# Kernel tuning notes

Hardware: AMD Instinct MI355X
Metric: run time of the kernel (lower is better)

The kernel has to match this reference:

```python
import jax, jax.numpy as jnp
import numpy as np

NU, NM = 100000, 20000   # users, merchants
FU, FM = 64, 32          # input feature dims
H = 128                  # hidden_channels
E = 1000000              # edges per edge type
ET = 500000              # target edges


def setup_inputs() -> dict:
    key = jax.random.key(0)
    ks = jax.random.split(key, 24)
    f = lambda i, shape: jax.random.normal(ks[i], shape, jnp.float32) * 0.05
    ri = lambda i, n, hi: jax.random.randint(ks[i], (n,), 0, hi)
    return {
        'x_user': f(0, (NU, FU)),
        'x_merchant': f(1, (NM, FM)),
        'row_um': ri(2, E, NU), 'col_um': ri(3, E, NM),
        'row_mu': ri(4, E, NM), 'col_mu': ri(5, E, NU),
        'row_t': ri(6, ET, NU), 'col_t': ri(7, ET, NM),
        'W1l_um': f(8, (FU, H)), 'W1r_um': f(9, (FM, H)), 'b1_um': jnp.zeros((H,), jnp.float32),
        'W1l_mu': f(10, (FM, H)), 'W1r_mu': f(11, (FU, H)), 'b1_mu': jnp.zeros((H,), jnp.float32),
        'W2l_um': f(12, (H, H)), 'W2r_um': f(13, (H, H)), 'b2_um': jnp.zeros((H,), jnp.float32),
        'W2l_mu': f(14, (H, H)), 'W2r_mu': f(15, (H, H)), 'b2_mu': jnp.zeros((H,), jnp.float32),
        'Wc1': f(16, (2 * H, H)), 'bc1': jnp.zeros((H,), jnp.float32),
        'Wc2': f(17, (H, 1)), 'bc2': jnp.zeros((1,), jnp.float32),
    }


def _sage(x_src, x_dst, row, col, Wl, Wr, b, n_dst):
    # PyG SAGEConv (aggr='mean'): lin_l(mean of neighbor msgs) + lin_r(root) + bias
    deg = jax.ops.segment_sum(jnp.ones(row.shape[0], x_src.dtype), col, num_segments=n_dst)
    agg = jax.ops.segment_sum(x_src[row], col, num_segments=n_dst)
    agg = agg / jnp.maximum(deg, 1.0)[:, None]
    return agg @ Wl + x_dst @ Wr + b


def reference(x_user, x_merchant, row_um, col_um, row_mu, col_mu, row_t, col_t,
              W1l_um, W1r_um, b1_um, W1l_mu, W1r_mu, b1_mu,
              W2l_um, W2r_um, b2_um, W2l_mu, W2r_mu, b2_mu,
              Wc1, bc1, Wc2, bc2):
    # Layer 1 (each dest type receives exactly one edge type -> hetero-mean is identity)
    h_m = jax.nn.relu(_sage(x_user, x_merchant, row_um, col_um, W1l_um, W1r_um, b1_um, NM))
    h_u = jax.nn.relu(_sage(x_merchant, x_user, row_mu, col_mu, W1l_mu, W1r_mu, b1_mu, NU))
    # Layer 2 (no activation)
    z_m = _sage(h_u, h_m, row_um, col_um, W2l_um, W2r_um, b2_um, NM)
    z_u = _sage(h_m, h_u, row_mu, col_mu, W2l_mu, W2r_mu, b2_mu, NU)
    # Edge classifier: gather sender ('user') / receiver ('merchant'), concat, MLP
    z = jnp.concatenate([z_u[row_t], z_m[col_t]], axis=-1)  # [ET, 2H]
    h = jax.nn.relu(z @ Wc1 + bc1)
    return (h @ Wc2 + bc2).reshape(-1)
```

## Files before the change

kernel.cpp:

```cpp
#include <hip/hip_runtime.h>
#include <hip/hip_bf16.h>

#define NUV 100000
#define NMV 20000
#define NEV 1000000
#define ETV 500000

#define CHK 8192
#define NCH 123
#define WNM 5000
#define WNU 25000
#define NCA 5
#define NCB 25
#define HGRID 1954
#define MBLK 5000
#define G1MB 625
#define G2MB 313

typedef unsigned short u16;
typedef unsigned int u32;
typedef __attribute__((ext_vector_type(8))) short s16x8;
typedef __attribute__((ext_vector_type(4))) float f32x4;
typedef __attribute__((ext_vector_type(4))) unsigned short u16x4;
typedef __attribute__((ext_vector_type(4))) unsigned int u32x4;

__device__ inline u16 bf16r(float f) {
  u32 b = __builtin_bit_cast(u32, f);
  u32 r = b + 0x7fffu + ((b >> 16) & 1u);
  return (u16)(r >> 16);
}
__device__ inline float bflo(u32 v) { return __builtin_bit_cast(float, v << 16); }
__device__ inline float bfhi(u32 v) { return __builtin_bit_cast(float, v & 0xffff0000u); }

#define GLOAD_LDS16(src, dst) \
  __builtin_amdgcn_global_load_lds((const __attribute__((address_space(1))) void*)(src), \
                                   (__attribute__((address_space(3))) void*)(dst), 16, 0, 0)

__global__ __launch_bounds__(512) void k_hist_lds(
    const int* __restrict__ col_um, u32* __restrict__ rankp_um, u32* __restrict__ cnt_um,
    const int* __restrict__ col_mu, u32* __restrict__ rankp_mu, u32* __restrict__ cnt_mu) {
  __shared__ u32 hist[WNU];
  int bid = blockIdx.x, tid = threadIdx.x;
  bool um = bid < NCH;
  const int* col = um ? col_um : col_mu;
  u32* rankp = um ? rankp_um : rankp_mu;
  u32* cntp = um ? cnt_um : cnt_mu;
  int Wn = um ? WNM : WNU;
  int blk = um ? bid : bid - NCH;
  int e0 = blk * CHK;
  for (int i = tid; i < Wn; i += 512) hist[i] = 0;
  __syncthreads();
  #pragma unroll
  for (int it = 0; it < CHK / 2048; ++it) {
    int li = e0 + (it * 512 + tid) * 4;
    if (li < NEV) {
      int4 c = *(const int4*)(col + li);
      int cc[4] = {c.x, c.y, c.z, c.w};
      u32 pk = 0;
      #pragma unroll
      for (int q = 0; q < 4; ++q) {
        int d = cc[q];
        int sh = 8 * (d & 3);
        u32 old = atomicAdd(&hist[d >> 2], 1u << sh);
        pk |= ((old >> sh) & 0xFFu) << (8 * q);
      }
      rankp[li >> 2] = pk;
    }
  }
  __syncthreads();
  u32* dst = cntp + (size_t)blk * Wn;
  for (int i = tid; i < Wn; i += 512) dst[i] = hist[i];
}

__global__ __launch_bounds__(1024) void k_scan_s1(
    const u32* __restrict__ cnt_um, u32* __restrict__ pre_um,
    const u32* __restrict__ cnt_mu, u32* __restrict__ pre_mu,
    int* __restrict__ T, int* __restrict__ bsum) {
  int b = blockIdx.x;
  const u32* cnt; u32* pre; int Wn; int w0; int* Tout;
  if (b < NCA) { cnt = cnt_um; pre = pre_um; Wn = WNM; w0 = b * 1024; Tout = T; }
  else         { cnt = cnt_mu; pre = pre_mu; Wn = WNU; w0 = (b - NCA) * 1024; Tout = T + NMV; }
  __shared__ int wsum[16];
  int tid = threadIdx.x, lane = tid & 63, w = tid >> 6;
  int wd = w0 + tid;
  int r0 = 0, r1 = 0, r2 = 0, r3 = 0;
  if (wd < Wn) {
    #pragma unroll 4
    for (int bb = 0; bb < NCH; ++bb) {
      u32 v = cnt[(size_t)bb * Wn + wd];
      pre[(size_t)bb * Wn + wd] =
          (u32)r0 | ((u32)r1 << 8) | ((u32)r2 << 16) | ((u32)r3 << 24);
      r0 += v & 0xFF; r1 += (v >> 8) & 0xFF; r2 += (v >> 16) & 0xFF; r3 += (v >> 24) & 0xFF;
    }
    *(int4*)(Tout + wd * 4) = make_int4(r0, r1, r2, r3);
  }
  int tot = r0 + r1 + r2 + r3;
  #pragma unroll
  for (int d = 1; d < 64; d <<= 1) tot += __shfl_xor(tot, d);
  if (lane == 0) wsum[w] = tot;
  __syncthreads();
  if (tid == 0) {
    int a = 0;
    #pragma unroll
    for (int j = 0; j < 16; ++j) a += wsum[j];
    bsum[b] = a;
  }
}

__global__ __launch_bounds__(128) void k_scan_s2(int* __restrict__ bsum,
                                                 int* __restrict__ off_um, int* __restrict__ off_mu) {
  int tid = threadIdx.x;
  int wv = tid >> 6, lane = tid & 63;
  if (wv == 0) {
    int v = (lane < NCA) ? bsum[lane] : 0;
    int s = v;
    #pragma unroll
    for (int d = 1; d < 64; d <<= 1) { int t = __shfl_up(s, d); if (lane >= d) s += t; }
    if (lane < NCA) bsum[lane] = s - v;
  } else {
    int v = (lane < NCB) ? bsum[NCA + lane] : 0;
    int s = v;
    #pragma unroll
    for (int d = 1; d < 64; d <<= 1) { int t = __shfl_up(s, d); if (lane >= d) s += t; }
    if (lane < NCB) bsum[NCA + lane] = s - v;
  }
  if (tid == 0) { off_um[NMV] = NEV; off_mu[NUV] = NEV; }
}

__global__ __launch_bounds__(1024) void k_scan_s3(int* __restrict__ off_um,
                                                  int* __restrict__ off_mu,
                                                  const int* __restrict__ T,
                                                  const int* __restrict__ bsum) {
  int b = blockIdx.x;
  int N; int c0; int* offo; const int* Tin;
  if (b < NCA) { N = NMV; c0 = b * 4096; offo = off_um; Tin = T; }
  else         { N = NUV; c0 = (b - NCA) * 4096; offo = off_mu; Tin = T + NMV; }
  int carry = bsum[b];
  __shared__ int wsum[16];
  int tid = threadIdx.x, lane = tid & 63, w = tid >> 6;
  int c = c0 + tid * 4;
  int4 tv = make_int4(0, 0, 0, 0);
  if (c < N) tv = *(const int4*)(Tin + c);
  int p1 = tv.x + tv.y, p2 = p1 + tv.z, p3 = p2 + tv.w;
  int sc = p3;
  #pragma unroll
  for (int d = 1; d < 64; d <<= 1) { int t = __shfl_up(sc, d); if (lane >= d) sc += t; }
  if (lane == 63) wsum[w] = sc;
  __syncthreads();
  if (w == 0 && lane < 16) {
    int ws_ = wsum[lane];
    #pragma unroll
    for (int d = 1; d < 16; d <<= 1) { int t = __shfl_up(ws_, d, 16); if (lane >= d) ws_ += t; }
    wsum[lane] = ws_;
  }
  __syncthreads();
  int ex = sc - p3 + (w ? wsum[w - 1] : 0) + carry;
  if (c < N) *(int4*)(offo + c) = make_int4(ex, ex + tv.x, ex + p1, ex + p2);
}

__global__ __launch_bounds__(256) void k_scatter3(
    const int* __restrict__ col_um, const int* __restrict__ row_um,
    const u32* __restrict__ rankp_um, const u32* __restrict__ pre_um,
    const int* __restrict__ off_um, int* __restrict__ srow_um,
    const int* __restrict__ col_mu, const int* __restrict__ row_mu,
    const u32* __restrict__ rankp_mu, const u32* __restrict__ pre_mu,
    const int* __restrict__ off_mu, int* __restrict__ srow_mu) {
  int i = (blockIdx.x * 256 + threadIdx.x) * 4;
  if (i >= 2 * NEV) return;
  bool um = i < NEV;
  const int* col = um ? col_um : col_mu;
  const int* row = um ? row_um : row_mu;
  const u32* rankp = um ? rankp_um : rankp_mu;
  const u32* pre = um ? pre_um : pre_mu;
  const int* off = um ? off_um : off_mu;
  int Wn = um ? WNM : WNU;
  int* srow = um ? srow_um : srow_mu;
  int lo = um ? i : i - NEV;
  int blk = lo >> 13;
  const u32* prep = pre + (size_t)blk * Wn;
  int4 c = *(const int4*)(col + lo);
  int4 rr = *(const int4*)(row + lo);
  u32 pk = rankp[lo >> 2];
  int cc[4] = {c.x, c.y, c.z, c.w}, rv[4] = {rr.x, rr.y, rr.z, rr.w};
  #pragma unroll
  for (int q = 0; q < 4; ++q) {
    int d = cc[q];
    int prefix = (int)((prep[d >> 2] >> (8 * (d & 3))) & 0xFF);
    int rank = (int)((pk >> (8 * q)) & 0xFF);
    srow[off[d] + prefix + rank] = rv[q];
  }
}

__global__ __launch_bounds__(256) void k_xub(const float* __restrict__ in, u32* __restrict__ o, int n8) {
  int stride = gridDim.x * 256;
  for (int i = blockIdx.x * 256 + threadIdx.x; i < n8; i += stride) {
    float4 a = *(const float4*)(in + (size_t)i * 8);
    float4 b = *(const float4*)(in + (size_t)i * 8 + 4);
    u32x4 r;
    r[0] = (u32)bf16r(a.x) | ((u32)bf16r(a.y) << 16);
    r[1] = (u32)bf16r(a.z) | ((u32)bf16r(a.w) << 16);
    r[2] = (u32)bf16r(b.x) | ((u32)bf16r(b.y) << 16);
    r[3] = (u32)bf16r(b.z) | ((u32)bf16r(b.w) << 16);
    *(u32x4*)(o + (size_t)i * 4) = r;
  }
}

__global__ __launch_bounds__(256) void k_agg_l1(
    const int* __restrict__ off_um, const int* __restrict__ srow_um,
    const u32* __restrict__ xub, float* __restrict__ agg_m,
    const int* __restrict__ off_mu, const int* __restrict__ srow_mu,
    const float* __restrict__ xm, float* __restrict__ agg_u) {
  int bid = blockIdx.x, tid = threadIdx.x;
  int l = tid & 63, g = l >> 3, lr = l & 7;
  if (bid < MBLK) {
    int wid = (bid * 256 + tid) >> 6;
    int s = off_um[wid], t = off_um[wid + 1];
    float a[8] = {};
    int j = s;
    for (; j + 16 <= t; j += 16) {
      int r0 = srow_um[j + g], r1 = srow_um[j + 8 + g];
      u32x4 v0 = *(const u32x4*)(xub + (size_t)r0 * 32 + lr * 4);
      u32x4 v1 = *(const u32x4*)(xub + (size_t)r1 * 32 + lr * 4);
      #pragma unroll
      for (int k = 0; k < 4; ++k) {
        a[2 * k] += bflo(v0[k]) + bflo(v1[k]);
        a[2 * k + 1] += bfhi(v0[k]) + bfhi(v1[k]);
      }
    }
    for (; j + 8 <= t; j += 8) {
      int r0 = srow_um[j + g];
      u32x4 v0 = *(const u32x4*)(xub + (size_t)r0 * 32 + lr * 4);
      #pragma unroll
      for (int k = 0; k < 4; ++k) { a[2 * k] += bflo(v0[k]); a[2 * k + 1] += bfhi(v0[k]); }
    }
    if (g < t - j) {
      int r0 = srow_um[j + g];
      u32x4 v0 = *(const u32x4*)(xub + (size_t)r0 * 32 + lr * 4);
      #pragma unroll
      for (int k = 0; k < 4; ++k) { a[2 * k] += bflo(v0[k]); a[2 * k + 1] += bfhi(v0[k]); }
    }
    #pragma unroll
    for (int k = 0; k < 8; ++k) {
      a[k] += __shfl_xor(a[k], 8);
      a[k] += __shfl_xor(a[k], 16);
      a[k] += __shfl_xor(a[k], 32);
    }
    if (g == 0) {
      float inv = 1.f / (float)max(t - s, 1);
      float4 o0 = make_float4(a[0] * inv, a[1] * inv, a[2] * inv, a[3] * inv);
      float4 o1 = make_float4(a[4] * inv, a[5] * inv, a[6] * inv, a[7] * inv);
      *(float4*)(agg_m + (size_t)wid * 64 + lr * 8) = o0;
      *(float4*)(agg_m + (size_t)wid * 64 + lr * 8 + 4) = o1;
    }
  } else {
    int wid = ((bid - MBLK) * 256 + tid) >> 6;
    int s = off_mu[wid], t = off_mu[wid + 1];
    float a[4] = {};
    int j = s;
    for (; j + 16 <= t; j += 16) {
      int r0 = srow_mu[j + g], r1 = srow_mu[j + 8 + g];
      float4 v0 = *(const float4*)(xm + (size_t)r0 * 32 + lr * 4);
      float4 v1 = *(const float4*)(xm + (size_t)r1 * 32 + lr * 4);
      a[0] += v0.x + v1.x; a[1] += v0.y + v1.y;
      a[2] += v0.z + v1.z; a[3] += v0.w + v1.w;
    }
    for (; j + 8 <= t; j += 8) {
      int r0 = srow_mu[j + g];
      float4 v0 = *(const float4*)(xm + (size_t)r0 * 32 + lr * 4);
      a[0] += v0.x; a[1] += v0.y; a[2] += v0.z; a[3] += v0.w;
    }
    if (g < t - j) {
      int r0 = srow_mu[j + g];
      float4 v0 = *(const float4*)(xm + (size_t)r0 * 32 + lr * 4);
      a[0] += v0.x; a[1] += v0.y; a[2] += v0.z; a[3] += v0.w;
    }
    #pragma unroll
    for (int k = 0; k < 4; ++k) {
      a[k] += __shfl_xor(a[k], 8);
      a[k] += __shfl_xor(a[k], 16);
      a[k] += __shfl_xor(a[k], 32);
    }
    if (g == 0) {
      float inv = 1.f / (float)max(t - s, 1);
      *(float4*)(agg_u + (size_t)wid * 32 + lr * 4) =
          make_float4(a[0] * inv, a[1] * inv, a[2] * inv, a[3] * inv);
    }
  }
}

__global__ __launch_bounds__(256) void k_agg_l2(
    const int* __restrict__ off_um, const int* __restrict__ srow_um,
    const u16* __restrict__ h_u, u16* __restrict__ aggb_m,
    const int* __restrict__ off_mu, const int* __restrict__ srow_mu,
    const u16* __restrict__ h_m, u16* __restrict__ aggb_u) {
  int bid = blockIdx.x, tid = threadIdx.x;
  const int* off; const int* srow; const u32* x; u32* ag; int wid;
  if (bid < MBLK) {
    off = off_um; srow = srow_um; x = (const u32*)h_u; ag = (u32*)aggb_m;
    wid = (bid * 256 + tid) >> 6;
  } else {
    off = off_mu; srow = srow_mu; x = (const u32*)h_m; ag = (u32*)aggb_u;
    wid = ((bid - MBLK) * 256 + tid) >> 6;
  }
  int l = tid & 63, g = l >> 4, lr = l & 15;
  int s = off[wid], t = off[wid + 1];
  float a[8] = {};
  int j = s;
  for (; j + 8 <= t; j += 8) {
    int r0 = srow[j + g], r1 = srow[j + 4 + g];
    u32x4 v0 = *(const u32x4*)(x + (size_t)r0 * 64 + lr * 4);
    u32x4 v1 = *(const u32x4*)(x + (size_t)r1 * 64 + lr * 4);
    #pragma unroll
    for (int k = 0; k < 4; ++k) {
      a[2 * k] += bflo(v0[k]) + bflo(v1[k]);
      a[2 * k + 1] += bfhi(v0[k]) + bfhi(v1[k]);
    }
  }
  for (; j + 4 <= t; j += 4) {
    int r0 = srow[j + g];
    u32x4 v0 = *(const u32x4*)(x + (size_t)r0 * 64 + lr * 4);
    #pragma unroll
    for (int k = 0; k < 4; ++k) { a[2 * k] += bflo(v0[k]); a[2 * k + 1] += bfhi(v0[k]); }
  }
  if (g < t - j) {
    int r0 = srow[j + g];
    u32x4 v0 = *(const u32x4*)(x + (size_t)r0 * 64 + lr * 4);
    #pragma unroll
    for (int k = 0; k < 4; ++k) { a[2 * k] += bflo(v0[k]); a[2 * k + 1] += bfhi(v0[k]); }
  }
  #pragma unroll
  for (int k = 0; k < 8; ++k) {
    a[k] += __shfl_xor(a[k], 16);
    a[k] += __shfl_xor(a[k], 32);
  }
  if (g == 0) {
    float inv = 1.f / (float)max(t - s, 1);
    u32x4 o;
    #pragma unroll
    for (int k = 0; k < 4; ++k)
      o[k] = (u32)bf16r(a[2 * k] * inv) | ((u32)bf16r(a[2 * k + 1] * inv) << 16);
    *(u32x4*)(ag + (size_t)wid * 64 + lr * 4) = o;
  }
}

template <int KA, int KB>
__device__ inline void gemm1_body(const float* __restrict__ A, const float* __restrict__ B,
                                  const float* __restrict__ Wa, const float* __restrict__ Wb,
                                  const float* __restrict__ bias, u16* __restrict__ outb,
                                  int m0, float* At, float* Bt) {
  int tid = threadIdx.x;
  {
    int m = tid & 31, kq = tid >> 5;
    const float* Ar = A + (size_t)(m0 + m) * KA;
    for (int k0 = kq * 4; k0 < KA; k0 += 32) {
      float4 v = *(const float4*)(Ar + k0);
      At[(k0 + 0) * 32 + m] = v.x; At[(k0 + 1) * 32 + m] = v.y;
      At[(k0 + 2) * 32 + m] = v.z; At[(k0 + 3) * 32 + m] = v.w;
    }
    const float* Br = B + (size_t)(m0 + m) * KB;
    for (int k0 = kq * 4; k0 < KB; k0 += 32) {
      float4 v = *(const float4*)(Br + k0);
      Bt[(k0 + 0) * 32 + m] = v.x; Bt[(k0 + 1) * 32 + m] = v.y;
      Bt[(k0 + 2) * 32 + m] = v.z; Bt[(k0 + 3) * 32 + m] = v.w;
    }
  }
  __syncthreads();
  int tx = tid & 31, ty = tid >> 5;
  float acc[4][4] = {};
  #pragma unroll 4
  for (int k = 0; k < KA; ++k) {
    float4 wv = *(const float4*)(Wa + k * 128 + tx * 4);
    float4 av = *(const float4*)(&At[k * 32 + ty * 4]);
    float am[4] = {av.x, av.y, av.z, av.w};
    float wo[4] = {wv.x, wv.y, wv.z, wv.w};
    #pragma unroll
    for (int mi = 0; mi < 4; ++mi)
      #pragma unroll
      for (int oi = 0; oi < 4; ++oi) acc[mi][oi] += am[mi] * wo[oi];
  }
  #pragma unroll 4
  for (int k = 0; k < KB; ++k) {
    float4 wv = *(const float4*)(Wb + k * 128 + tx * 4);
    float4 av = *(const float4*)(&Bt[k * 32 + ty * 4]);
    float am[4] = {av.x, av.y, av.z, av.w};
    float wo[4] = {wv.x, wv.y, wv.z, wv.w};
    #pragma unroll
    for (int mi = 0; mi < 4; ++mi)
      #pragma unroll
      for (int oi = 0; oi < 4; ++oi) acc[mi][oi] += am[mi] * wo[oi];
  }
  float4 bv = *(const float4*)(bias + tx * 4);
  float bb[4] = {bv.x, bv.y, bv.z, bv.w};
  #pragma unroll
  for (int mi = 0; mi < 4; ++mi) {
    u16x4 o;
    #pragma unroll
    for (int oi = 0; oi < 4; ++oi) {
      float v = acc[mi][oi] + bb[oi];
      v = v > 0.f ? v : 0.f;
      o[oi] = bf16r(v);
    }
    *(u16x4*)(outb + (size_t)(m0 + ty * 4 + mi) * 128 + tx * 4) = o;
  }
}

__global__ __launch_bounds__(256) void k_gemm1(
    const float* __restrict__ agg_m, const float* __restrict__ x_merch,
    const float* __restrict__ W1l_um, const float* __restrict__ W1r_um,
    const float* __restrict__ b1_um, u16* __restrict__ h_m,
    const float* __restrict__ agg_u, const float* __restrict__ x_user,
    const float* __restrict__ W1l_mu, const float* __restrict__ W1r_mu,
    const float* __restrict__ b1_mu, u16* __restrict__ h_u) {
  __shared__ float At[64 * 32];
  __shared__ float Bt[64 * 32];
  int bid = blockIdx.x;
  if (bid < G1MB)
    gemm1_body<64, 32>(agg_m, x_merch, W1l_um, W1r_um, b1_um, h_m, bid * 32, At, Bt);
  else
    gemm1_body<32, 64>(agg_u, x_user, W1l_mu, W1r_mu, b1_mu, h_u, (bid - G1MB) * 32, At, Bt);
}

__global__ __launch_bounds__(256) void k_prep_comb(
    const float* __restrict__ W2l_um, const float* __restrict__ W2r_um,
    const float* __restrict__ W2l_mu, const float* __restrict__ W2r_mu,
    const float* __restrict__ b2_um, const float* __restrict__ b2_mu,
    const float* __restrict__ Wc1, const float* __restrict__ bc1,
    u16* __restrict__ WtA_u, u16* __restrict__ WtB_u,
    u16* __restrict__ WtA_m, u16* __restrict__ WtB_m,
    float* __restrict__ bias_u, float* __restrict__ bias_m) {
  int t = blockIdx.x * 256 + threadIdx.x;
  if (t < 65536) {
    int mat = t >> 14, rem = t & 16383;
    int o = rem >> 7, k = rem & 127;
    const float* W2 = mat == 0 ? W2l_mu : mat == 1 ? W2r_mu : mat == 2 ? W2l_um : W2r_um;
    const float* wc = Wc1 + (mat >= 2 ? 128 * 128 : 0) + o;
    float s = 0.f;
    #pragma unroll 4
    for (int j = 0; j < 128; ++j) s += W2[k * 128 + j] * wc[j * 128];
    u16* dst = mat == 0 ? WtA_u : mat == 1 ? WtB_u : mat == 2 ? WtA_m : WtB_m;
    dst[o * 128 + k] = bf16r(s);
  } else if (t < 65536 + 256) {
    int r = t - 65536;
    int o = r & 127;
    if (r < 128) {
      float s = 0.f;
      for (int j = 0; j < 128; ++j) s += b2_mu[j] * Wc1[j * 128 + o];
      bias_u[o] = s;
    } else {
      float s = bc1[o];
      for (int j = 0; j < 128; ++j) s += b2_um[j] * Wc1[(128 + j) * 128 + o];
      bias_m[o] = s;
    }
  }
}

__global__ __launch_bounds__(256) void k_gemm2_mfma(
    const u16* __restrict__ aggb_m, const u16* __restrict__ h_m,
    const u16* __restrict__ WtA_m, const u16* __restrict__ WtB_m,
    const float* __restrict__ bias_m, u16* __restrict__ pm_b,
    const u16* __restrict__ aggb_u, const u16* __restrict__ h_u,
    const u16* __restrict__ WtA_u, const u16* __restrict__ WtB_u,
    const float* __restrict__ bias_u, u16* __restrict__ pu_b) {
  __shared__ u16 Zs[64 * 256];
  int tid = threadIdx.x;
  int bid = blockIdx.x;
  const u16 *aggb, *hb, *Wtl, *Wtr; const float* bias; u16* zb; int nd, r0;
  if (bid < G2MB) {
    aggb = aggb_m; hb = h_m; Wtl = WtA_m; Wtr = WtB_m; bias = bias_m; zb = pm_b;
    nd = NMV; r0 = bid * 64;
  } else {
    aggb = aggb_u; hb = h_u; Wtl = WtA_u; Wtr = WtB_u; bias = bias_u; zb = pu_b;
    nd = NUV; r0 = (bid - G2MB) * 64;
  }
  {
    int half = (tid >> 4) & 1;
    const u16* tab = half ? hb : aggb;
    #pragma unroll
    for (int it = 0; it < 8; ++it) {
      int q = tid + it * 256;
      int rl = q >> 5;
      int cc = (q & 15) ^ (rl & 7);
      int r = r0 + rl; r = r < nd ? r : nd - 1;
      const u16* src = tab + (size_t)r * 128 + cc * 8;
      u16* dst = Zs + (tid >> 6) * 512 + it * 2048;
      GLOAD_LDS16(src, dst);
    }
  }
  __syncthreads();
  int l = tid & 63, wv = tid >> 6;
  int lg = l >> 4, lr = l & 15;
  f32x4 acc[4][2];
  #pragma unroll
  for (int mt = 0; mt < 4; ++mt)
    #pragma unroll
    for (int c = 0; c < 2; ++c) acc[mt][c] = (f32x4){0.f, 0.f, 0.f, 0.f};
  #pragma unroll
  for (int cti = 0; cti < 2; ++cti) {
    int o = (wv * 2 + cti) * 16 + lr;
    const u16* wpl = Wtl + (size_t)o * 128 + lg * 8;
    const u16* wpr = Wtr + (size_t)o * 128 + lg * 8;
    s16x8 b[8];
    #pragma unroll
    for (int ks = 0; ks < 4; ++ks) b[ks] = *(const s16x8*)(wpl + ks * 32);
    #pragma unroll
    for (int ks = 0; ks < 4; ++ks) b[ks + 4] = *(const s16x8*)(wpr + ks * 32);
    #pragma unroll
    for (int mt = 0; mt < 4; ++mt) {
      int rl = mt * 16 + lr;
      int rb = rl * 512, sw = (rl & 7) << 4;
      #pragma unroll
      for (int ks = 0; ks < 8; ++ks) {
        s16x8 a = *(const s16x8*)((const char*)Zs + ((rb + ks * 64 + lg * 16) ^ sw));
        acc[mt][cti] = __builtin_amdgcn_mfma_f32_16x16x32_bf16(a, b[ks], acc[mt][cti], 0, 0, 0);
      }
    }
  }
  float bv[2];
  #pragma unroll
  for (int cti = 0; cti < 2; ++cti) bv[cti] = bias[(wv * 2 + cti) * 16 + lr];
  #pragma unroll
  for (int mt = 0; mt < 4; ++mt)
    #pragma unroll
    for (int cti = 0; cti < 2; ++cti) {
      int o = (wv * 2 + cti) * 16 + lr;
      #pragma unroll
      for (int rg = 0; rg < 4; ++rg) {
        int r = r0 + mt * 16 + lg * 4 + rg;
        if (r < nd) zb[(size_t)r * 128 + o] = bf16r(acc[mt][cti][rg] + bv[cti]);
      }
    }
}

__global__ __launch_bounds__(256) void k_edge(
    const u32* __restrict__ pu, const u32* __restrict__ pm,
    const int* __restrict__ row_t, const int* __restrict__ col_t,
    const float* __restrict__ Wc2, const float* __restrict__ bc2,
    float* __restrict__ out) {
  __shared__ float res[256];
  int tid = threadIdx.x, l = tid & 63, wv = tid >> 6;
  int lr = l & 15, g = l >> 4;
  float w2v[8];
  #pragma unroll
  for (int q = 0; q < 8; ++q) w2v[q] = Wc2[lr * 8 + q];
  int base = blockIdx.x * 256 + wv * 64;
  #pragma unroll 2
  for (int it = 0; it < 16; ++it) {
    int e = base + it * 4 + g;
    int ec = e < ETV ? e : ETV - 1;
    int r = row_t[ec], c = col_t[ec];
    u32x4 a = *(const u32x4*)(pu + (size_t)r * 64 + lr * 4);
    u32x4 b = *(const u32x4*)(pm + (size_t)c * 64 + lr * 4);
    float p = 0.f;
    #pragma unroll
    for (int q = 0; q < 4; ++q) {
      float h0 = bflo(a[q]) + bflo(b[q]);
      float h1 = bfhi(a[q]) + bfhi(b[q]);
      h0 = h0 > 0.f ? h0 : 0.f;
      h1 = h1 > 0.f ? h1 : 0.f;
      p += h0 * w2v[2 * q] + h1 * w2v[2 * q + 1];
    }
    p += __shfl_xor(p, 1); p += __shfl_xor(p, 2);
    p += __shfl_xor(p, 4); p += __shfl_xor(p, 8);
    if (lr == 0) res[wv * 64 + it * 4 + g] = p;
  }
  __syncthreads();
  int eo = blockIdx.x * 256 + tid;
  if (eo < ETV) out[eo] = res[tid] + bc2[0];
}

extern "C" void kernel_launch(void* const* d_in, const int* in_sizes, int n_in,
                              void* d_out, int out_size, void* d_ws, size_t ws_size,
                              hipStream_t stream) {
  const float* x_user  = (const float*)d_in[0];
  const float* x_merch = (const float*)d_in[1];
  const int* row_um = (const int*)d_in[2]; const int* col_um = (const int*)d_in[3];
  const int* row_mu = (const int*)d_in[4]; const int* col_mu = (const int*)d_in[5];
  const int* row_t  = (const int*)d_in[6]; const int* col_t  = (const int*)d_in[7];
  const float* W1l_um = (const float*)d_in[8];  const float* W1r_um = (const float*)d_in[9];  const float* b1_um = (const float*)d_in[10];
  const float* W1l_mu = (const float*)d_in[11]; const float* W1r_mu = (const float*)d_in[12]; const float* b1_mu = (const float*)d_in[13];
  const float* W2l_um = (const float*)d_in[14]; const float* W2r_um = (const float*)d_in[15]; const float* b2_um = (const float*)d_in[16];
  const float* W2l_mu = (const float*)d_in[17]; const float* W2r_mu = (const float*)d_in[18]; const float* b2_mu = (const float*)d_in[19];
  const float* Wc1 = (const float*)d_in[20]; const float* bc1 = (const float*)d_in[21];
  const float* Wc2 = (const float*)d_in[22]; const float* bc2 = (const float*)d_in[23];
  float* out = (float*)d_out;

  char* ws = (char*)d_ws;
  size_t p = 0;
  auto alloc = [&](size_t bytes) -> char* {
    char* r = ws + p;
    p = (p + bytes + 255) & ~(size_t)255;
    return r;
  };
  u32* cnt_um = (u32*)alloc((size_t)NCH * WNM * 4);
  u32* cnt_mu = (u32*)alloc((size_t)NCH * WNU * 4);
  u32* pre_um = (u32*)alloc((size_t)NCH * WNM * 4);
  u32* pre_mu = (u32*)alloc((size_t)NCH * WNU * 4);
  u32* rankp_um = (u32*)alloc((size_t)(NEV / 4) * 4);
  u32* rankp_mu = (u32*)alloc((size_t)(NEV / 4) * 4);
  int* off_um = (int*)alloc((size_t)(NMV + 4) * 4);
  int* off_mu = (int*)alloc((size_t)(NUV + 4) * 4);
  int* T    = (int*)alloc((size_t)(NMV + NUV) * 4);
  int* bsum = (int*)alloc((size_t)(NCA + NCB) * 4);
  int* srow_um = (int*)alloc((size_t)NEV * 4);
  int* srow_mu = (int*)alloc((size_t)NEV * 4);
  u32* xub = (u32*)alloc((size_t)NUV * 32 * 4);
  float* agg_m = (float*)alloc((size_t)NMV * 64 * 4);
  float* agg_u = (float*)alloc((size_t)NUV * 32 * 4);
  u16* h_m   = (u16*)alloc((size_t)NMV * 128 * 2);
  u16* h_u   = (u16*)alloc((size_t)NUV * 128 * 2);
  u16* aggb_m = (u16*)alloc((size_t)NMV * 128 * 2);
  u16* aggb_u = (u16*)alloc((size_t)NUV * 128 * 2);
  u16* pm_b  = (u16*)alloc((size_t)NMV * 128 * 2);
  u16* pu_b  = (u16*)alloc((size_t)NUV * 128 * 2);
  u16* WtA_u = (u16*)alloc((size_t)128 * 128 * 2);
  u16* WtB_u = (u16*)alloc((size_t)128 * 128 * 2);
  u16* WtA_m = (u16*)alloc((size_t)128 * 128 * 2);
  u16* WtB_m = (u16*)alloc((size_t)128 * 128 * 2);
  float* bias_u = (float*)alloc(128 * 4);
  float* bias_m = (float*)alloc(128 * 4);
  if (p > ws_size) return;

  k_prep_comb<<<257, 256, 0, stream>>>(W2l_um, W2r_um, W2l_mu, W2r_mu, b2_um, b2_mu, Wc1, bc1,
                                       WtA_u, WtB_u, WtA_m, WtB_m, bias_u, bias_m);
  k_xub<<<1024, 256, 0, stream>>>(x_user, xub, NUV * 64 / 8);
  k_hist_lds<<<2 * NCH, 512, 0, stream>>>(col_um, rankp_um, cnt_um,
                                          col_mu, rankp_mu, cnt_mu);
  k_scan_s1<<<NCA + NCB, 1024, 0, stream>>>(cnt_um, pre_um, cnt_mu, pre_mu, T, bsum);
  k_scan_s2<<<1, 128, 0, stream>>>(bsum, off_um, off_mu);
  k_scan_s3<<<NCA + NCB, 1024, 0, stream>>>(off_um, off_mu, T, bsum);
  k_scatter3<<<HGRID, 256, 0, stream>>>(col_um, row_um, rankp_um, pre_um, off_um, srow_um,
                                        col_mu, row_mu, rankp_mu, pre_mu, off_mu, srow_mu);
  k_agg_l1<<<MBLK + NUV / 4, 256, 0, stream>>>(off_um, srow_um, xub, agg_m,
                                               off_mu, srow_mu, x_merch, agg_u);
  k_gemm1<<<G1MB + NUV / 32, 256, 0, stream>>>(agg_m, x_merch, W1l_um, W1r_um, b1_um, h_m,
                                               agg_u, x_user, W1l_mu, W1r_mu, b1_mu, h_u);
  k_agg_l2<<<MBLK + NUV / 4, 256, 0, stream>>>(off_um, srow_um, h_u, aggb_m,
                                               off_mu, srow_mu, h_m, aggb_u);
  k_gemm2_mfma<<<G2MB + (NUV + 63) / 64, 256, 0, stream>>>(
      aggb_m, h_m, WtA_m, WtB_m, bias_m, pm_b,
      aggb_u, h_u, WtA_u, WtB_u, bias_u, pu_b);
  k_edge<<<(ETV + 255) / 256, 256, 0, stream>>>((const u32*)pu_b, (const u32*)pm_b,
                                                row_t, col_t, Wc2, bc2, out);
}
```

Before: 336.9 us.

## Use bf16 MFMA for layer-1 SAGE GEMM over a concatenated aggregate/root buffer

Layer 1 now packs the mean aggregate and the root features side by side in one bf16 row-major buffer per node type (zero-padded to 128 columns). A single MFMA GEMM runs against a combined, transposed bf16 weight, replacing the fp32 FMA GEMM that read two separate fp32 inputs. The aggregation kernels now read bf16 merchant features and write bf16 outputs straight into the concat buffer. Gather loops in both aggregation layers are unrolled to four loads in flight. The change adds bf16 rounding of the merchant features and the layer-1 aggregates, plus wasted padded-K work in the GEMM.

```diff
diff --git a/kernel.cpp b/kernel.cpp
--- a/kernel.cpp
+++ b/kernel.cpp
@@ -14,14 +14,14 @@
 #define NCB 25
 #define HGRID 1954
 #define MBLK 5000
-#define G1MB 625
+#define G1TM 313
 #define G2MB 313
 
 typedef unsigned short u16;
 typedef unsigned int u32;
 typedef __attribute__((ext_vector_type(8))) short s16x8;
 typedef __attribute__((ext_vector_type(4))) float f32x4;
-typedef __attribute__((ext_vector_type(4))) unsigned short u16x4;
+typedef __attribute__((ext_vector_type(2))) unsigned int u32x2;
 typedef __attribute__((ext_vector_type(4))) unsigned int u32x4;
 
 __device__ inline u16 bf16r(float f) {
@@ -191,242 +191,16 @@
   }
 }
 
-__global__ __launch_bounds__(256) void k_xub(const float* __restrict__ in, u32* __restrict__ o, int n8) {
-  int stride = gridDim.x * 256;
-  for (int i = blockIdx.x * 256 + threadIdx.x; i < n8; i += stride) {
-    float4 a = *(const float4*)(in + (size_t)i * 8);
-    float4 b = *(const float4*)(in + (size_t)i * 8 + 4);
-    u32x4 r;
-    r[0] = (u32)bf16r(a.x) | ((u32)bf16r(a.y) << 16);
-    r[1] = (u32)bf16r(a.z) | ((u32)bf16r(a.w) << 16);
-    r[2] = (u32)bf16r(b.x) | ((u32)bf16r(b.y) << 16);
-    r[3] = (u32)bf16r(b.z) | ((u32)bf16r(b.w) << 16);
-    *(u32x4*)(o + (size_t)i * 4) = r;
-  }
-}
-
-__global__ __launch_bounds__(256) void k_agg_l1(
-    const int* __restrict__ off_um, const int* __restrict__ srow_um,
-    const u32* __restrict__ xub, float* __restrict__ agg_m,
-    const int* __restrict__ off_mu, const int* __restrict__ srow_mu,
-    const float* __restrict__ xm, float* __restrict__ agg_u) {
-  int bid = blockIdx.x, tid = threadIdx.x;
-  int l = tid & 63, g = l >> 3, lr = l & 7;
-  if (bid < MBLK) {
-    int wid = (bid * 256 + tid) >> 6;
-    int s = off_um[wid], t = off_um[wid + 1];
-    float a[8] = {};
-    int j = s;
-    for (; j + 16 <= t; j += 16) {
-      int r0 = srow_um[j + g], r1 = srow_um[j + 8 + g];
-      u32x4 v0 = *(const u32x4*)(xub + (size_t)r0 * 32 + lr * 4);
-      u32x4 v1 = *(const u32x4*)(xub + (size_t)r1 * 32 + lr * 4);
-      #pragma unroll
-      for (int k = 0; k < 4; ++k) {
-        a[2 * k] += bflo(v0[k]) + bflo(v1[k]);
-        a[2 * k + 1] += bfhi(v0[k]) + bfhi(v1[k]);
-      }
-    }
-    for (; j + 8 <= t; j += 8) {
-      int r0 = srow_um[j + g];
-      u32x4 v0 = *(const u32x4*)(xub + (size_t)r0 * 32 + lr * 4);
-      #pragma unroll
-      for (int k = 0; k < 4; ++k) { a[2 * k] += bflo(v0[k]); a[2 * k + 1] += bfhi(v0[k]); }
-    }
-    if (g < t - j) {
-      int r0 = srow_um[j + g];
-      u32x4 v0 = *(const u32x4*)(xub + (size_t)r0 * 32 + lr * 4);
-      #pragma unroll
-      for (int k = 0; k < 4; ++k) { a[2 * k] += bflo(v0[k]); a[2 * k + 1] += bfhi(v0[k]); }
-    }
-    #pragma unroll
-    for (int k = 0; k < 8; ++k) {
-      a[k] += __shfl_xor(a[k], 8);
-      a[k] += __shfl_xor(a[k], 16);
-      a[k] += __shfl_xor(a[k], 32);
-    }
-    if (g == 0) {
-      float inv = 1.f / (float)max(t - s, 1);
-      float4 o0 = make_float4(a[0] * inv, a[1] * inv, a[2] * inv, a[3] * inv);
-      float4 o1 = make_float4(a[4] * inv, a[5] * inv, a[6] * inv, a[7] * inv);
-      *(float4*)(agg_m + (size_t)wid * 64 + lr * 8) = o0;
-      *(float4*)(agg_m + (size_t)wid * 64 + lr * 8 + 4) = o1;
-    }
-  } else {
-    int wid = ((bid - MBLK) * 256 + tid) >> 6;
-    int s = off_mu[wid], t = off_mu[wid + 1];
-    float a[4] = {};
-    int j = s;
-    for (; j + 16 <= t; j += 16) {
-      int r0 = srow_mu[j + g], r1 = srow_mu[j + 8 + g];
-      float4 v0 = *(const float4*)(xm + (size_t)r0 * 32 + lr * 4);
-      float4 v1 = *(const float4*)(xm + (size_t)r1 * 32 + lr * 4);
-      a[0] += v0.x + v1.x; a[1] += v0.y + v1.y;
-      a[2] += v0.z + v1.z; a[3] += v0.w + v1.w;
-    }
-    for (; j + 8 <= t; j += 8) {
-      int r0 = srow_mu[j + g];
-      float4 v0 = *(const float4*)(xm + (size_t)r0 * 32 + lr * 4);
-      a[0] += v0.x; a[1] += v0.y; a[2] += v0.z; a[3] += v0.w;
-    }
-    if (g < t - j) {
-      int r0 = srow_mu[j + g];
-      float4 v0 = *(const float4*)(xm + (size_t)r0 * 32 + lr * 4);
-      a[0] += v0.x; a[1] += v0.y; a[2] += v0.z; a[3] += v0.w;
-    }
-    #pragma unroll
-    for (int k = 0; k < 4; ++k) {
-      a[k] += __shfl_xor(a[k], 8);
-      a[k] += __shfl_xor(a[k], 16);
-      a[k] += __shfl_xor(a[k], 32);
-    }
-    if (g == 0) {
-      float inv = 1.f / (float)max(t - s, 1);
-      *(float4*)(agg_u + (size_t)wid * 32 + lr * 4) =
-          make_float4(a[0] * inv, a[1] * inv, a[2] * inv, a[3] * inv);
-    }
-  }
-}
-
-__global__ __launch_bounds__(256) void k_agg_l2(
-    const int* __restrict__ off_um, const int* __restrict__ srow_um,
-    const u16* __restrict__ h_u, u16* __restrict__ aggb_m,
-    const int* __restrict__ off_mu, const int* __restrict__ srow_mu,
-    const u16* __restrict__ h_m, u16* __restrict__ aggb_u) {
-  int bid = blockIdx.x, tid = threadIdx.x;
-  const int* off; const int* srow; const u32* x; u32* ag; int wid;
-  if (bid < MBLK) {
-    off = off_um; srow = srow_um; x = (const u32*)h_u; ag = (u32*)aggb_m;
-    wid = (bid * 256 + tid) >> 6;
-  } else {
-    off = off_mu; srow = srow_mu; x = (const u32*)h_m; ag = (u32*)aggb_u;
-    wid = ((bid - MBLK) * 256 + tid) >> 6;
-  }
-  int l = tid & 63, g = l >> 4, lr = l & 15;
-  int s = off[wid], t = off[wid + 1];
-  float a[8] = {};
-  int j = s;
-  for (; j + 8 <= t; j += 8) {
-    int r0 = srow[j + g], r1 = srow[j + 4 + g];
-    u32x4 v0 = *(const u32x4*)(x + (size_t)r0 * 64 + lr * 4);
-    u32x4 v1 = *(const u32x4*)(x + (size_t)r1 * 64 + lr * 4);
-    #pragma unroll
-    for (int k = 0; k < 4; ++k) {
-      a[2 * k] += bflo(v0[k]) + bflo(v1[k]);
-      a[2 * k + 1] += bfhi(v0[k]) + bfhi(v1[k]);
-    }
-  }
-  for (; j + 4 <= t; j += 4) {
-    int r0 = srow[j + g];
-    u32x4 v0 = *(const u32x4*)(x + (size_t)r0 * 64 + lr * 4);
-    #pragma unroll
-    for (int k = 0; k < 4; ++k) { a[2 * k] += bflo(v0[k]); a[2 * k + 1] += bfhi(v0[k]); }
-  }
-  if (g < t - j) {
-    int r0 = srow[j + g];
-    u32x4 v0 = *(const u32x4*)(x + (size_t)r0 * 64 + lr * 4);
-    #pragma unroll
-    for (int k = 0; k < 4; ++k) { a[2 * k] += bflo(v0[k]); a[2 * k + 1] += bfhi(v0[k]); }
-  }
-  #pragma unroll
-  for (int k = 0; k < 8; ++k) {
-    a[k] += __shfl_xor(a[k], 16);
-    a[k] += __shfl_xor(a[k], 32);
-  }
-  if (g == 0) {
-    float inv = 1.f / (float)max(t - s, 1);
-    u32x4 o;
-    #pragma unroll
-    for (int k = 0; k < 4; ++k)
-      o[k] = (u32)bf16r(a[2 * k] * inv) | ((u32)bf16r(a[2 * k + 1] * inv) << 16);
-    *(u32x4*)(ag + (size_t)wid * 64 + lr * 4) = o;
-  }
-}
-
-template <int KA, int KB>
-__device__ inline void gemm1_body(const float* __restrict__ A, const float* __restrict__ B,
-                                  const float* __restrict__ Wa, const float* __restrict__ Wb,
-                                  const float* __restrict__ bias, u16* __restrict__ outb,
-                                  int m0, float* At, float* Bt) {
-  int tid = threadIdx.x;
-  {
-    int m = tid & 31, kq = tid >> 5;
-    const float* Ar = A + (size_t)(m0 + m) * KA;
-    for (int k0 = kq * 4; k0 < KA; k0 += 32) {
-      float4 v = *(const float4*)(Ar + k0);
-      At[(k0 + 0) * 32 + m] = v.x; At[(k0 + 1) * 32 + m] = v.y;
-      At[(k0 + 2) * 32 + m] = v.z; At[(k0 + 3) * 32 + m] = v.w;
-    }
-    const float* Br = B + (size_t)(m0 + m) * KB;
-    for (int k0 = kq * 4; k0 < KB; k0 += 32) {
-      float4 v = *(const float4*)(Br + k0);
-      Bt[(k0 + 0) * 32 + m] = v.x; Bt[(k0 + 1) * 32 + m] = v.y;
-      Bt[(k0 + 2) * 32 + m] = v.z; Bt[(k0 + 3) * 32 + m] = v.w;
-    }
-  }
-  __syncthreads();
-  int tx = tid & 31, ty = tid >> 5;
-  float acc[4][4] = {};
-  #pragma unroll 4
-  for (int k = 0; k < KA; ++k) {
-    float4 wv = *(const float4*)(Wa + k * 128 + tx * 4);
-    float4 av = *(const float4*)(&At[k * 32 + ty * 4]);
-    float am[4] = {av.x, av.y, av.z, av.w};
-    float wo[4] = {wv.x, wv.y, wv.z, wv.w};
-    #pragma unroll
-    for (int mi = 0; mi < 4; ++mi)
-      #pragma unroll
-      for (int oi = 0; oi < 4; ++oi) acc[mi][oi] += am[mi] * wo[oi];
-  }
-  #pragma unroll 4
-  for (int k = 0; k < KB; ++k) {
-    float4 wv = *(const float4*)(Wb + k * 128 + tx * 4);
-    float4 av = *(const float4*)(&Bt[k * 32 + ty * 4]);
-    float am[4] = {av.x, av.y, av.z, av.w};
-    float wo[4] = {wv.x, wv.y, wv.z, wv.w};
-    #pragma unroll
-    for (int mi = 0; mi < 4; ++mi)
-      #pragma unroll
-      for (int oi = 0; oi < 4; ++oi) acc[mi][oi] += am[mi] * wo[oi];
-  }
-  float4 bv = *(const float4*)(bias + tx * 4);
-  float bb[4] = {bv.x, bv.y, bv.z, bv.w};
-  #pragma unroll
-  for (int mi = 0; mi < 4; ++mi) {
-    u16x4 o;
-    #pragma unroll
-    for (int oi = 0; oi < 4; ++oi) {
-      float v = acc[mi][oi] + bb[oi];
-      v = v > 0.f ? v : 0.f;
-      o[oi] = bf16r(v);
-    }
-    *(u16x4*)(outb + (size_t)(m0 + ty * 4 + mi) * 128 + tx * 4) = o;
-  }
-}
-
-__global__ __launch_bounds__(256) void k_gemm1(
-    const float* __restrict__ agg_m, const float* __restrict__ x_merch,
+__global__ __launch_bounds__(256) void k_prep_w(
     const float* __restrict__ W1l_um, const float* __restrict__ W1r_um,
-    const float* __restrict__ b1_um, u16* __restrict__ h_m,
-    const float* __restrict__ agg_u, const float* __restrict__ x_user,
     const float* __restrict__ W1l_mu, const float* __restrict__ W1r_mu,
-    const float* __restrict__ b1_mu, u16* __restrict__ h_u) {
-  __shared__ float At[64 * 32];
-  __shared__ float Bt[64 * 32];
-  int bid = blockIdx.x;
-  if (bid < G1MB)
-    gemm1_body<64, 32>(agg_m, x_merch, W1l_um, W1r_um, b1_um, h_m, bid * 32, At, Bt);
-  else
-    gemm1_body<32, 64>(agg_u, x_user, W1l_mu, W1r_mu, b1_mu, h_u, (bid - G1MB) * 32, At, Bt);
-}
-
-__global__ __launch_bounds__(256) void k_prep_comb(
     const float* __restrict__ W2l_um, const float* __restrict__ W2r_um,
     const float* __restrict__ W2l_mu, const float* __restrict__ W2r_mu,
     const float* __restrict__ b2_um, const float* __restrict__ b2_mu,
     const float* __restrict__ Wc1, const float* __restrict__ bc1,
     u16* __restrict__ WtA_u, u16* __restrict__ WtB_u,
     u16* __restrict__ WtA_m, u16* __restrict__ WtB_m,
+    u16* __restrict__ Wt1_m, u16* __restrict__ Wt1_u,
     float* __restrict__ bias_u, float* __restrict__ bias_m) {
   int t = blockIdx.x * 256 + threadIdx.x;
   if (t < 65536) {
@@ -451,6 +225,276 @@
       for (int j = 0; j < 128; ++j) s += b2_um[j] * Wc1[(128 + j) * 128 + o];
       bias_m[o] = s;
     }
+  } else if (t < 65792 + 32768) {
+    int idx = t - 65792;
+    int mat = idx >> 14, rem = idx & 16383;
+    int o = rem >> 7, k = rem & 127;
+    if (mat == 0) {
+      float v = k < 64 ? W1l_um[k * 128 + o] : (k < 96 ? W1r_um[(k - 64) * 128 + o] : 0.f);
+      Wt1_m[o * 128 + k] = bf16r(v);
+    } else {
+      float v = k < 32 ? W1l_mu[k * 128 + o] : (k < 96 ? W1r_mu[(k - 32) * 128 + o] : 0.f);
+      Wt1_u[o * 128 + k] = bf16r(v);
+    }
+  }
+}
+
+__global__ __launch_bounds__(256) void k_prep_x(
+    const float* __restrict__ x_user, const float* __restrict__ x_merch,
+    u32* __restrict__ cat_u, u32* __restrict__ cat_m) {
+  int id = blockIdx.x * 256 + threadIdx.x;
+  if (id < NUV * 12) {
+    int row = id / 12, wg = id % 12;
+    if (wg < 8) {
+      const float* src = x_user + (size_t)row * 64 + wg * 8;
+      float4 a = *(const float4*)src, b = *(const float4*)(src + 4);
+      u32x4 r;
+      r[0] = (u32)bf16r(a.x) | ((u32)bf16r(a.y) << 16);
+      r[1] = (u32)bf16r(a.z) | ((u32)bf16r(a.w) << 16);
+      r[2] = (u32)bf16r(b.x) | ((u32)bf16r(b.y) << 16);
+      r[3] = (u32)bf16r(b.z) | ((u32)bf16r(b.w) << 16);
+      *(u32x4*)(cat_u + (size_t)row * 64 + 16 + wg * 4) = r;
+    } else {
+      *(u32x4*)(cat_u + (size_t)row * 64 + 48 + (wg - 8) * 4) = (u32x4){0, 0, 0, 0};
+    }
+  } else if (id < NUV * 12 + NMV * 8) {
+    int id2 = id - NUV * 12;
+    int row = id2 / 8, wg = id2 % 8;
+    if (wg < 4) {
+      const float* src = x_merch + (size_t)row * 32 + wg * 8;
+      float4 a = *(const float4*)src, b = *(const float4*)(src + 4);
+      u32x4 r;
+      r[0] = (u32)bf16r(a.x) | ((u32)bf16r(a.y) << 16);
+      r[1] = (u32)bf16r(a.z) | ((u32)bf16r(a.w) << 16);
+      r[2] = (u32)bf16r(b.x) | ((u32)bf16r(b.y) << 16);
+      r[3] = (u32)bf16r(b.z) | ((u32)bf16r(b.w) << 16);
+      *(u32x4*)(cat_m + (size_t)row * 64 + 32 + wg * 4) = r;
+    } else {
+      *(u32x4*)(cat_m + (size_t)row * 64 + 48 + (wg - 4) * 4) = (u32x4){0, 0, 0, 0};
+    }
+  }
+}
+
+__global__ __launch_bounds__(256) void k_agg_l1(
+    const int* __restrict__ off_um, const int* __restrict__ srow_um,
+    const int* __restrict__ off_mu, const int* __restrict__ srow_mu,
+    u32* __restrict__ cat_u, u32* __restrict__ cat_m) {
+  int bid = blockIdx.x, tid = threadIdx.x;
+  int l = tid & 63, g = l >> 3, lr = l & 7;
+  if (bid < MBLK) {
+    int wid = (bid * 256 + tid) >> 6;
+    int s = off_um[wid], t = off_um[wid + 1];
+    const u32* gx = cat_u;
+    float a[8] = {};
+    int j = s;
+    for (; j + 32 <= t; j += 32) {
+      int r0 = srow_um[j + g], r1 = srow_um[j + 8 + g];
+      int r2 = srow_um[j + 16 + g], r3 = srow_um[j + 24 + g];
+      u32x4 v0 = *(const u32x4*)(gx + (size_t)r0 * 64 + 16 + lr * 4);
+      u32x4 v1 = *(const u32x4*)(gx + (size_t)r1 * 64 + 16 + lr * 4);
+      u32x4 v2 = *(const u32x4*)(gx + (size_t)r2 * 64 + 16 + lr * 4);
+      u32x4 v3 = *(const u32x4*)(gx + (size_t)r3 * 64 + 16 + lr * 4);
+      #pragma unroll
+      for (int k = 0; k < 4; ++k) {
+        a[2 * k] += (bflo(v0[k]) + bflo(v1[k])) + (bflo(v2[k]) + bflo(v3[k]));
+        a[2 * k + 1] += (bfhi(v0[k]) + bfhi(v1[k])) + (bfhi(v2[k]) + bfhi(v3[k]));
+      }
+    }
+    for (; j + 8 <= t; j += 8) {
+      int r0 = srow_um[j + g];
+      u32x4 v0 = *(const u32x4*)(gx + (size_t)r0 * 64 + 16 + lr * 4);
+      #pragma unroll
+      for (int k = 0; k < 4; ++k) { a[2 * k] += bflo(v0[k]); a[2 * k + 1] += bfhi(v0[k]); }
+    }
+    if (g < t - j) {
+      int r0 = srow_um[j + g];
+      u32x4 v0 = *(const u32x4*)(gx + (size_t)r0 * 64 + 16 + lr * 4);
+      #pragma unroll
+      for (int k = 0; k < 4; ++k) { a[2 * k] += bflo(v0[k]); a[2 * k + 1] += bfhi(v0[k]); }
+    }
+    #pragma unroll
+    for (int k = 0; k < 8; ++k) {
+      a[k] += __shfl_xor(a[k], 8);
+      a[k] += __shfl_xor(a[k], 16);
+      a[k] += __shfl_xor(a[k], 32);
+    }
+    if (g == 0) {
+      float inv = 1.f / (float)max(t - s, 1);
+      u32x4 o;
+      #pragma unroll
+      for (int k = 0; k < 4; ++k)
+        o[k] = (u32)bf16r(a[2 * k] * inv) | ((u32)bf16r(a[2 * k + 1] * inv) << 16);
+      *(u32x4*)(cat_m + (size_t)wid * 64 + lr * 4) = o;
+    }
+  } else {
+    int wid = ((bid - MBLK) * 256 + tid) >> 6;
+    int s = off_mu[wid], t = off_mu[wid + 1];
+    const u32* gx = cat_m;
+    float a[4] = {};
+    int j = s;
+    for (; j + 32 <= t; j += 32) {
+      int r0 = srow_mu[j + g], r1 = srow_mu[j + 8 + g];
+      int r2 = srow_mu[j + 16 + g], r3 = srow_mu[j + 24 + g];
+      u32x2 v0 = *(const u32x2*)(gx + (size_t)r0 * 64 + 32 + lr * 2);
+      u32x2 v1 = *(const u32x2*)(gx + (size_t)r1 * 64 + 32 + lr * 2);
+      u32x2 v2 = *(const u32x2*)(gx + (size_t)r2 * 64 + 32 + lr * 2);
+      u32x2 v3 = *(const u32x2*)(gx + (size_t)r3 * 64 + 32 + lr * 2);
+      #pragma unroll
+      for (int k = 0; k < 2; ++k) {
+        a[2 * k] += (bflo(v0[k]) + bflo(v1[k])) + (bflo(v2[k]) + bflo(v3[k]));
+        a[2 * k + 1] += (bfhi(v0[k]) + bfhi(v1[k])) + (bfhi(v2[k]) + bfhi(v3[k]));
+      }
+    }
+    for (; j + 8 <= t; j += 8) {
+      int r0 = srow_mu[j + g];
+      u32x2 v0 = *(const u32x2*)(gx + (size_t)r0 * 64 + 32 + lr * 2);
+      #pragma unroll
+      for (int k = 0; k < 2; ++k) { a[2 * k] += bflo(v0[k]); a[2 * k + 1] += bfhi(v0[k]); }
+    }
+    if (g < t - j) {
+      int r0 = srow_mu[j + g];
+      u32x2 v0 = *(const u32x2*)(gx + (size_t)r0 * 64 + 32 + lr * 2);
+      #pragma unroll
+      for (int k = 0; k < 2; ++k) { a[2 * k] += bflo(v0[k]); a[2 * k + 1] += bfhi(v0[k]); }
+    }
+    #pragma unroll
+    for (int k = 0; k < 4; ++k) {
+      a[k] += __shfl_xor(a[k], 8);
+      a[k] += __shfl_xor(a[k], 16);
+      a[k] += __shfl_xor(a[k], 32);
+    }
+    if (g == 0) {
+      float inv = 1.f / (float)max(t - s, 1);
+      u32x2 o;
+      #pragma unroll
+      for (int k = 0; k < 2; ++k)
+        o[k] = (u32)bf16r(a[2 * k] * inv) | ((u32)bf16r(a[2 * k + 1] * inv) << 16);
+      *(u32x2*)(cat_u + (size_t)wid * 64 + lr * 2) = o;
+    }
+  }
+}
+
+__global__ __launch_bounds__(256) void k_gemm1_mfma(
+    const u16* __restrict__ cat_m, const u16* __restrict__ Wt1_m,
+    const float* __restrict__ b1_um, u16* __restrict__ h_m,
+    const u16* __restrict__ cat_u, const u16* __restrict__ Wt1_u,
+    const float* __restrict__ b1_mu, u16* __restrict__ h_u) {
+  __shared__ u16 Zs[64 * 128];
+  int tid = threadIdx.x, bid = blockIdx.x;
+  const u16 *cat, *Wt; const float* bias; u16* ho; int nd, r0;
+  if (bid < G1TM) { cat = cat_m; Wt = Wt1_m; bias = b1_um; ho = h_m; nd = NMV; r0 = bid * 64; }
+  else { cat = cat_u; Wt = Wt1_u; bias = b1_mu; ho = h_u; nd = NUV; r0 = (bid - G1TM) * 64; }
+  #pragma unroll
+  for (int it = 0; it < 4; ++it) {
+    int q = tid + it * 256;
+    int rl = q >> 4;
+    int cc = (q & 15) ^ (rl & 7);
+    int r = r0 + rl; r = r < nd ? r : nd - 1;
+    const u16* src = cat + (size_t)r * 128 + cc * 8;
+    u16* dst = Zs + (tid >> 6) * 512 + it * 2048;
+    GLOAD_LDS16(src, dst);
+  }
+  __syncthreads();
+  int l = tid & 63, wv = tid >> 6;
+  int lg = l >> 4, lr = l & 15;
+  f32x4 acc[4][2];
+  #pragma unroll
+  for (int mt = 0; mt < 4; ++mt)
+    #pragma unroll
+    for (int c = 0; c < 2; ++c) acc[mt][c] = (f32x4){0.f, 0.f, 0.f, 0.f};
+  #pragma unroll
+  for (int cti = 0; cti < 2; ++cti) {
+    int o = (wv * 2 + cti) * 16 + lr;
+    const u16* wp = Wt + (size_t)o * 128 + lg * 8;
+    s16x8 b[4];
+    #pragma unroll
+    for (int ks = 0; ks < 4; ++ks) b[ks] = *(const s16x8*)(wp + ks * 32);
+    #pragma unroll
+    for (int mt = 0; mt < 4; ++mt) {
+      int rl = mt * 16 + lr;
+      int rb = rl * 256, sw = (rl & 7) << 4;
+      #pragma unroll
+      for (int ks = 0; ks < 4; ++ks) {
+        s16x8 a = *(const s16x8*)((const char*)Zs + ((rb + ks * 64 + lg * 16) ^ sw));
+        acc[mt][cti] = __builtin_amdgcn_mfma_f32_16x16x32_bf16(a, b[ks], acc[mt][cti], 0, 0, 0);
+      }
+    }
+  }
+  float bv[2];
+  #pragma unroll
+  for (int cti = 0; cti < 2; ++cti) bv[cti] = bias[(wv * 2 + cti) * 16 + lr];
+  #pragma unroll
+  for (int mt = 0; mt < 4; ++mt)
+    #pragma unroll
+    for (int cti = 0; cti < 2; ++cti) {
+      int o = (wv * 2 + cti) * 16 + lr;
+      #pragma unroll
+      for (int rg = 0; rg < 4; ++rg) {
+        int r = r0 + mt * 16 + lg * 4 + rg;
+        if (r < nd) {
+          float v = acc[mt][cti][rg] + bv[cti];
+          v = v > 0.f ? v : 0.f;
+          ho[(size_t)r * 128 + o] = bf16r(v);
+        }
+      }
+    }
+}
+
+__global__ __launch_bounds__(256) void k_agg_l2(
+    const int* __restrict__ off_um, const int* __restrict__ srow_um,
+    const u16* __restrict__ h_u, u16* __restrict__ aggb_m,
+    const int* __restrict__ off_mu, const int* __restrict__ srow_mu,
+    const u16* __restrict__ h_m, u16* __restrict__ aggb_u) {
+  int bid = blockIdx.x, tid = threadIdx.x;
+  const int* off; const int* srow; const u32* x; u32* ag; int wid;
+  if (bid < MBLK) {
+    off = off_um; srow = srow_um; x = (const u32*)h_u; ag = (u32*)aggb_m;
+    wid = (bid * 256 + tid) >> 6;
+  } else {
+    off = off_mu; srow = srow_mu; x = (const u32*)h_m; ag = (u32*)aggb_u;
+    wid = ((bid - MBLK) * 256 + tid) >> 6;
+  }
+  int l = tid & 63, g = l >> 4, lr = l & 15;
+  int s = off[wid], t = off[wid + 1];
+  float a[8] = {};
+  int j = s;
+  for (; j + 16 <= t; j += 16) {
+    int r0 = srow[j + g], r1 = srow[j + 4 + g];
+    int r2 = srow[j + 8 + g], r3 = srow[j + 12 + g];
+    u32x4 v0 = *(const u32x4*)(x + (size_t)r0 * 64 + lr * 4);
+    u32x4 v1 = *(const u32x4*)(x + (size_t)r1 * 64 + lr * 4);
+    u32x4 v2 = *(const u32x4*)(x + (size_t)r2 * 64 + lr * 4);
+    u32x4 v3 = *(const u32x4*)(x + (size_t)r3 * 64 + lr * 4);
+    #pragma unroll
+    for (int k = 0; k < 4; ++k) {
+      a[2 * k] += (bflo(v0[k]) + bflo(v1[k])) + (bflo(v2[k]) + bflo(v3[k]));
+      a[2 * k + 1] += (bfhi(v0[k]) + bfhi(v1[k])) + (bfhi(v2[k]) + bfhi(v3[k]));
+    }
+  }
+  for (; j + 4 <= t; j += 4) {
+    int r0 = srow[j + g];
+    u32x4 v0 = *(const u32x4*)(x + (size_t)r0 * 64 + lr * 4);
+    #pragma unroll
+    for (int k = 0; k < 4; ++k) { a[2 * k] += bflo(v0[k]); a[2 * k + 1] += bfhi(v0[k]); }
+  }
+  if (g < t - j) {
+    int r0 = srow[j + g];
+    u32x4 v0 = *(const u32x4*)(x + (size_t)r0 * 64 + lr * 4);
+    #pragma unroll
+    for (int k = 0; k < 4; ++k) { a[2 * k] += bflo(v0[k]); a[2 * k + 1] += bfhi(v0[k]); }
+  }
+  #pragma unroll
+  for (int k = 0; k < 8; ++k) {
+    a[k] += __shfl_xor(a[k], 16);
+    a[k] += __shfl_xor(a[k], 32);
+  }
+  if (g == 0) {
+    float inv = 1.f / (float)max(t - s, 1);
+    u32x4 o;
+    #pragma unroll
+    for (int k = 0; k < 4; ++k)
+      o[k] = (u32)bf16r(a[2 * k] * inv) | ((u32)bf16r(a[2 * k + 1] * inv) << 16);
+    *(u32x4*)(ag + (size_t)wid * 64 + lr * 4) = o;
   }
 }
 
@@ -603,9 +647,8 @@
   int* bsum = (int*)alloc((size_t)(NCA + NCB) * 4);
   int* srow_um = (int*)alloc((size_t)NEV * 4);
   int* srow_mu = (int*)alloc((size_t)NEV * 4);
-  u32* xub = (u32*)alloc((size_t)NUV * 32 * 4);
-  float* agg_m = (float*)alloc((size_t)NMV * 64 * 4);
-  float* agg_u = (float*)alloc((size_t)NUV * 32 * 4);
+  u16* cat_m = (u16*)alloc((size_t)NMV * 128 * 2);
+  u16* cat_u = (u16*)alloc((size_t)NUV * 128 * 2);
   u16* h_m   = (u16*)alloc((size_t)NMV * 128 * 2);
   u16* h_u   = (u16*)alloc((size_t)NUV * 128 * 2);
   u16* aggb_m = (u16*)alloc((size_t)NMV * 128 * 2);
@@ -616,13 +659,17 @@
   u16* WtB_u = (u16*)alloc((size_t)128 * 128 * 2);
   u16* WtA_m = (u16*)alloc((size_t)128 * 128 * 2);
   u16* WtB_m = (u16*)alloc((size_t)128 * 128 * 2);
+  u16* Wt1_m = (u16*)alloc((size_t)128 * 128 * 2);
+  u16* Wt1_u = (u16*)alloc((size_t)128 * 128 * 2);
   float* bias_u = (float*)alloc(128 * 4);
   float* bias_m = (float*)alloc(128 * 4);
   if (p > ws_size) return;
 
-  k_prep_comb<<<257, 256, 0, stream>>>(W2l_um, W2r_um, W2l_mu, W2r_mu, b2_um, b2_mu, Wc1, bc1,
-                                       WtA_u, WtB_u, WtA_m, WtB_m, bias_u, bias_m);
-  k_xub<<<1024, 256, 0, stream>>>(x_user, xub, NUV * 64 / 8);
+  k_prep_w<<<386, 256, 0, stream>>>(W1l_um, W1r_um, W1l_mu, W1r_mu,
+                                    W2l_um, W2r_um, W2l_mu, W2r_mu, b2_um, b2_mu, Wc1, bc1,
+                                    WtA_u, WtB_u, WtA_m, WtB_m, Wt1_m, Wt1_u, bias_u, bias_m);
+  k_prep_x<<<(NUV * 12 + NMV * 8 + 255) / 256, 256, 0, stream>>>(x_user, x_merch,
+                                                                 (u32*)cat_u, (u32*)cat_m);
   k_hist_lds<<<2 * NCH, 512, 0, stream>>>(col_um, rankp_um, cnt_um,
                                           col_mu, rankp_mu, cnt_mu);
   k_scan_s1<<<NCA + NCB, 1024, 0, stream>>>(cnt_um, pre_um, cnt_mu, pre_mu, T, bsum);
@@ -630,10 +677,10 @@
   k_scan_s3<<<NCA + NCB, 1024, 0, stream>>>(off_um, off_mu, T, bsum);
   k_scatter3<<<HGRID, 256, 0, stream>>>(col_um, row_um, rankp_um, pre_um, off_um, srow_um,
                                         col_mu, row_mu, rankp_mu, pre_mu, off_mu, srow_mu);
-  k_agg_l1<<<MBLK + NUV / 4, 256, 0, stream>>>(off_um, srow_um, xub, agg_m,
-                                               off_mu, srow_mu, x_merch, agg_u);
-  k_gemm1<<<G1MB + NUV / 32, 256, 0, stream>>>(agg_m, x_merch, W1l_um, W1r_um, b1_um, h_m,
-                                               agg_u, x_user, W1l_mu, W1r_mu, b1_mu, h_u);
+  k_agg_l1<<<MBLK + NUV / 4, 256, 0, stream>>>(off_um, srow_um, off_mu, srow_mu,
+                                               (u32*)cat_u, (u32*)cat_m);
+  k_gemm1_mfma<<<G1TM + (NUV + 63) / 64, 256, 0, stream>>>(cat_m, Wt1_m, b1_um, h_m,
+                                                           cat_u, Wt1_u, b1_mu, h_u);
   k_agg_l2<<<MBLK + NUV / 4, 256, 0, stream>>>(off_um, srow_um, h_u, aggb_m,
                                                off_mu, srow_mu, h_m, aggb_u);
   k_gemm2_mfma<<<G2MB + (NUV + 63) / 64, 256, 0, stream>>>(
```

After: 322.5 us. 1.04x faster.
